# Kernel tuning notes

Measured on AMD Instinct MI355X. Metric: run time of the kernel, lower is better.

The kernel has to match this reference:

```python
import jax, jax.numpy as jnp
import numpy as np

EPS = 1e-12
FINAL_GROUPS = 256  # 4*64
FINAL_BIAS = 8.0


def resilu(x):
    # ReSiLU at default hardness == soft sigmoid gate
    return jax.nn.sigmoid(x)


def popcnt_layer(x, sel, w, b):
    # x: [B, In], sel: [O, P] int, w: [O, P], b: [O]
    selected = jnp.take(x, sel, axis=1)          # [B, O, P] gather
    weighted = selected * resilu(w)[None, :, :]  # weighted multiply
    summed = weighted.sum(axis=-1)               # [B, O] segment sum
    return resilu(summed - b[None, :])


def layer_norm(x, g, b):
    mu = x.mean(axis=-1, keepdims=True)
    var = ((x - mu) ** 2).mean(axis=-1, keepdims=True)
    return (x - mu) * jax.lax.rsqrt(var + EPS) * g + b


def setup_inputs() -> dict:
    key = jax.random.key(0)
    ks = jax.random.split(key, 16)
    B, IN, O1, O3, P = 256, 3200, 8192, 4096, 128
    return {
        "x": jax.random.normal(ks[0], (B, IN), dtype=jnp.float32),
        "sel1": jax.random.randint(ks[1], (O1, P), 0, IN, dtype=jnp.int32),
        "w1": jax.random.normal(ks[2], (O1, P), dtype=jnp.float32),
        "b1": jax.random.normal(ks[3], (O1,), dtype=jnp.float32) * (P / 3) + (P / 4),
        "g1": jnp.ones((O1,), dtype=jnp.float32),
        "be1": jnp.zeros((O1,), dtype=jnp.float32),
        "sel2": jax.random.randint(ks[4], (O1, P), 0, O1, dtype=jnp.int32),
        "w2": jax.random.normal(ks[5], (O1, P), dtype=jnp.float32),
        "b2": jax.random.normal(ks[6], (O1,), dtype=jnp.float32) * (P / 3) + (P / 4),
        "g2": jnp.ones((O1,), dtype=jnp.float32),
        "be2": jnp.zeros((O1,), dtype=jnp.float32),
        "sel3": jax.random.randint(ks[7], (O3, P), 0, O1, dtype=jnp.int32),
        "w3": jax.random.normal(ks[8], (O3, P), dtype=jnp.float32),
        "b3": jax.random.normal(ks[9], (O3,), dtype=jnp.float32) * (P / 3) + (P / 4),
    }


def reference(x, sel1, w1, b1, g1, be1, sel2, w2, b2, g2, be2, sel3, w3, b3):
    h = popcnt_layer(x, sel1, w1, b1)
    h = layer_norm(h, g1, be1)
    h = popcnt_layer(h, sel2, w2, b2)
    h = layer_norm(h, g2, be2)
    h = popcnt_layer(h, sel3, w3, b3)          # [B, 4096]
    out = h.reshape(h.shape[0], FINAL_GROUPS, -1).sum(axis=-1) - FINAL_BIAS  # [B, 256]
    return out
```

## Files before the change

kernel.cpp:

```cpp
#include <hip/hip_runtime.h>
#include <hip/hip_fp16.h>
#include <stdint.h>

#define BATCH 256
#define PSEL  128
#define IN_DIM 3200
#define O1_DIM 8192
#define O3_DIM 4096

__global__ __launch_bounds__(256) void transpose_kernel(const float* __restrict__ x,
                                                        __half* __restrict__ xT,
                                                        float* __restrict__ stats) {
    int tx = threadIdx.x;
    int ty = threadIdx.y;
    int tid = ty * 32 + tx;
    int gid = blockIdx.y * gridDim.x + blockIdx.x;
    if (gid < 4) stats[gid * 256 + tid] = 0.0f;

    __shared__ float tile[32][33];
    int i0 = blockIdx.x * 32;
    int b0 = blockIdx.y * 32;
#pragma unroll
    for (int k = 0; k < 4; ++k)
        tile[ty + k * 8][tx] =
            __builtin_nontemporal_load(&x[(size_t)(b0 + ty + k * 8) * IN_DIM + i0 + tx]);
    __syncthreads();
#pragma unroll
    for (int k = 0; k < 4; ++k)
        xT[(size_t)(i0 + ty + k * 8) * BATCH + b0 + tx] =
            __float2half(tile[tx][ty + k * 8]);
}

__global__ __launch_bounds__(256) void stats_kernel(const __half* __restrict__ hT,
                                                    float* __restrict__ gsum,
                                                    float* __restrict__ gsq) {
    int t   = threadIdx.x;
    int col = t & 127;
    int rp  = t >> 7;
    int r0  = blockIdx.x * 256 + rp * 128;
    const uint32_t* p = (const uint32_t*)hT + (size_t)r0 * 128 + col;
    float s0 = 0.f, s1 = 0.f, q0 = 0.f, q1 = 0.f;
#pragma unroll
    for (int ob = 0; ob < 16; ++ob) {
        uint32_t d[8];
#pragma unroll
        for (int j = 0; j < 8; ++j) d[j] = p[(size_t)(ob * 8 + j) * 128];
#pragma unroll
        for (int j = 0; j < 8; ++j) {
            float2 f = __half22float2(*(const __half2*)&d[j]);
            s0 += f.x; q0 = fmaf(f.x, f.x, q0);
            s1 += f.y; q1 = fmaf(f.y, f.y, q1);
        }
    }
    __shared__ float4 s_red[128];
    if (rp == 1) s_red[col] = make_float4(s0, s1, q0, q1);
    __syncthreads();
    if (rp == 0) {
        float4 r = s_red[col];
        atomicAdd(&gsum[2 * col],     s0 + r.x);
        atomicAdd(&gsum[2 * col + 1], s1 + r.y);
        atomicAdd(&gsq[2 * col],      q0 + r.z);
        atomicAdd(&gsq[2 * col + 1],  q1 + r.w);
    }
}

template <bool NORM>
__global__ __launch_bounds__(256, 4) void popcnt_kernel(
    const __half* __restrict__ actT,
    const int* __restrict__ sel,
    const float* __restrict__ w,
    const float* __restrict__ bias,
    const float* __restrict__ g,
    const float* __restrict__ be,
    const float* __restrict__ gsum,
    const float* __restrict__ gsq,
    float inv_n,
    __half* __restrict__ outp)
{
    const int o  = blockIdx.x;
    const int t  = threadIdx.x;
    const int cw = t & 31;
    const int rg = t >> 5;

    __shared__ uint32_t s_off[PSEL];
    __shared__ float    s_A[PSEL];
    __shared__ float s_rA[PSEL], s_rC[PSEL];
    __shared__ float s_acc[8][264];
    __shared__ float s_sums[2];

    if (t < PSEL) {
        int idx  = __builtin_nontemporal_load(&sel[o * PSEL + t]);
        float ww = __builtin_nontemporal_load(&w[o * PSEL + t]);
        float sw = 1.0f / (1.0f + __expf(-ww));
        float a, c;
        if (NORM) { a = sw * g[idx]; c = sw * be[idx]; }
        else      { a = sw;          c = 0.0f; }
        s_off[t] = (uint32_t)idx << 9;
        s_A[t]   = a;
        if (NORM) { s_rA[t] = a; s_rC[t] = c; }
    }
    __syncthreads();

    if (NORM && t < 64) {
        float va = s_rA[t] + s_rA[t + 64];
        float vc = s_rC[t] + s_rC[t + 64];
#pragma unroll
        for (int off = 32; off > 0; off >>= 1) {
            va += __shfl_down(va, off, 64);
            vc += __shfl_down(vc, off, 64);
        }
        if (t == 0) { s_sums[0] = va; s_sums[1] = vc; }
    }

    const uint32_t lane_off = (uint32_t)(cw << 4);
    uint32_t voff[16];
#pragma unroll
    for (int j = 0; j < 16; ++j)
        voff[j] = s_off[j * 8 + rg] + lane_off;
    uint4 d[16];
#pragma unroll
    for (int j = 0; j < 16; ++j)
        asm volatile("global_load_dwordx4 %0, %1, %2 sc0"
                     : "=v"(d[j])
                     : "v"(voff[j]), "s"(actT)
                     : "memory");
    asm volatile("s_waitcnt vmcnt(0)" ::: "memory");
    __builtin_amdgcn_sched_barrier(0);

    float acc[8] = {0.f, 0.f, 0.f, 0.f, 0.f, 0.f, 0.f, 0.f};
#pragma unroll
    for (int j = 0; j < 16; ++j) {
        float A = s_A[j * 8 + rg];
        const __half2* hp = (const __half2*)&d[j];
        float2 f0 = __half22float2(hp[0]);
        float2 f1 = __half22float2(hp[1]);
        float2 f2 = __half22float2(hp[2]);
        float2 f3 = __half22float2(hp[3]);
        acc[0] = fmaf(A, f0.x, acc[0]);
        acc[1] = fmaf(A, f0.y, acc[1]);
        acc[2] = fmaf(A, f1.x, acc[2]);
        acc[3] = fmaf(A, f1.y, acc[3]);
        acc[4] = fmaf(A, f2.x, acc[4]);
        acc[5] = fmaf(A, f2.y, acc[5]);
        acc[6] = fmaf(A, f3.x, acc[6]);
        acc[7] = fmaf(A, f3.y, acc[7]);
    }

    *(float4*)&s_acc[rg][8 * cw]     = make_float4(acc[0], acc[1], acc[2], acc[3]);
    *(float4*)&s_acc[rg][8 * cw + 4] = make_float4(acc[4], acc[5], acc[6], acc[7]);
    __syncthreads();

    float ab = 0.0f;
#pragma unroll
    for (int r = 0; r < 8; ++r) ab += s_acc[r][t];

    float bo = bias[o];
    float z;
    if (NORM) {
        float m  = gsum[t] * inv_n;
        float q  = gsq[t] * inv_n;
        float rs = rsqrtf(q - m * m + 1e-12f);
        z = rs * ab + s_sums[1] - rs * m * s_sums[0] - bo;
    } else {
        z = ab - bo;
    }
    float h = 1.0f / (1.0f + __expf(-z));
    __builtin_nontemporal_store(__half_as_ushort(__float2half(h)),
                                (unsigned short*)outp + (size_t)o * BATCH + t);
}

__global__ __launch_bounds__(256) void final_reduce(const __half* __restrict__ h3T,
                                                    float* __restrict__ out) {
    int gidx = blockIdx.x;
    int b    = threadIdx.x;
    const unsigned short* p = (const unsigned short*)h3T + (size_t)gidx * 16 * BATCH + b;
    float s = -8.0f;
#pragma unroll
    for (int j = 0; j < 16; ++j)
        s += __half2float(__ushort_as_half(__builtin_nontemporal_load(p + j * BATCH)));
    __builtin_nontemporal_store(s, &out[(size_t)b * 256 + gidx]);
}

extern "C" void kernel_launch(void* const* d_in, const int* in_sizes, int n_in,
                              void* d_out, int out_size, void* d_ws, size_t ws_size,
                              hipStream_t stream) {
    const float* x    = (const float*)d_in[0];
    const int*   sel1 = (const int*)d_in[1];
    const float* w1   = (const float*)d_in[2];
    const float* b1   = (const float*)d_in[3];
    const float* g1   = (const float*)d_in[4];
    const float* be1  = (const float*)d_in[5];
    const int*   sel2 = (const int*)d_in[6];
    const float* w2   = (const float*)d_in[7];
    const float* b2   = (const float*)d_in[8];
    const float* g2   = (const float*)d_in[9];
    const float* be2  = (const float*)d_in[10];
    const int*   sel3 = (const int*)d_in[11];
    const float* w3   = (const float*)d_in[12];
    const float* b3   = (const float*)d_in[13];
    float* out = (float*)d_out;

    char* ws = (char*)d_ws;
    __half* xT  = (__half*)(ws);
    __half* h1T = (__half*)(ws + 1638400);
    __half* h2T = (__half*)(ws + 1638400 + 4194304);
    __half* h3T = h1T;
    float* stats = (float*)(ws + 1638400 + 2 * 4194304);
    float* gs1 = stats;
    float* gq1 = stats + 256;
    float* gs2 = stats + 512;
    float* gq2 = stats + 768;

    transpose_kernel<<<dim3(IN_DIM / 32, BATCH / 32), dim3(32, 8), 0, stream>>>(
        x, xT, stats);

    popcnt_kernel<false><<<O1_DIM, 256, 0, stream>>>(
        xT, sel1, w1, b1, nullptr, nullptr, nullptr, nullptr, 0.0f, h1T);

    stats_kernel<<<O1_DIM / 256, 256, 0, stream>>>(h1T, gs1, gq1);

    popcnt_kernel<true><<<O1_DIM, 256, 0, stream>>>(
        h1T, sel2, w2, b2, g1, be1, gs1, gq1, 1.0f / (float)O1_DIM, h2T);

    stats_kernel<<<O1_DIM / 256, 256, 0, stream>>>(h2T, gs2, gq2);

    popcnt_kernel<true><<<O3_DIM, 256, 0, stream>>>(
        h2T, sel3, w3, b3, g2, be2, gs2, gq2, 1.0f / (float)O1_DIM, h3T);

    final_reduce<<<256, 256, 0, stream>>>(h3T, out);
}
```

Baseline: 182.4 us.

## Stage batch-slab activation tables in LDS for layers 2 and 3

Layers 2 and 3 now use a new kernel that copies a 128KB slab of the activation table (8 batch columns across all 8192 features) into LDS and gathers from shared memory instead of global/L2. A pack kernel precomputes the folded layer-norm weights (sigmoid(w)*g), byte offsets and per-output bias/shift metadata once. Activations are stored in a batch-blocked layout, and stats are computed per slab without atomics. This removes the repeated random global gathers and trades them for large LDS use (low occupancy), extra pack and relayout passes, and more workspace.

After: 233.7 us. 1.28x slower.

```diff
diff --git a/kernel.cpp b/kernel.cpp
--- a/kernel.cpp
+++ b/kernel.cpp
@@ -7,6 +7,13 @@
 #define IN_DIM 3200
 #define O1_DIM 8192
 #define O3_DIM 4096
+
+typedef unsigned int u32x4 __attribute__((ext_vector_type(4)));
+
+static __device__ inline uint32_t pack_half2(float a, float b) {
+    __half2 h = __floats2half2_rn(a, b);
+    return *reinterpret_cast<uint32_t*>(&h);
+}
 
 __global__ __launch_bounds__(256) void transpose_kernel(const float* __restrict__ x,
                                                         __half* __restrict__ xT,
@@ -31,7 +38,44 @@
             __float2half(tile[tx][ty + k * 8]);
 }
 
+__global__ __launch_bounds__(256) void pack_kernel(
+    const int* __restrict__ sel, const float* __restrict__ w,
+    const float* __restrict__ g, const float* __restrict__ be,
+    const float* __restrict__ bias,
+    uint2* __restrict__ pack, float2* __restrict__ meta) {
+    const int t = threadIdx.x;
+    const int slot = t >> 7;
+    const int e = t & 127;
+    const int o0 = blockIdx.x * 16;
+    __shared__ float s_p[4][2];
+    for (int k = 0; k < 8; ++k) {
+        int o = o0 + 2 * k + slot;
+        int idx  = sel[(size_t)o * PSEL + e];
+        float wv = w[(size_t)o * PSEL + e];
+        float sw = 1.0f / (1.0f + __expf(-wv));
+        float A = sw * g[idx];
+        float C = sw * be[idx];
+        pack[(size_t)o * PSEL + e] = make_uint2((uint32_t)idx << 4, __float_as_uint(A));
+        float va = A, vc = C;
+#pragma unroll
+        for (int off = 32; off > 0; off >>= 1) {
+            va += __shfl_down(va, off, 64);
+            vc += __shfl_down(vc, off, 64);
+        }
+        if ((t & 63) == 0) { s_p[t >> 6][0] = va; s_p[t >> 6][1] = vc; }
+        __syncthreads();
+        if (t < 2) {
+            float sA = s_p[2 * t][0] + s_p[2 * t + 1][0];
+            float sC = s_p[2 * t][1] + s_p[2 * t + 1][1];
+            int oo = o0 + 2 * k + t;
+            meta[oo] = make_float2(sA, sC - bias[oo]);
+        }
+        __syncthreads();
+    }
+}
+
 __global__ __launch_bounds__(256) void stats_kernel(const __half* __restrict__ hT,
+                                                    __half* __restrict__ hblk,
                                                     float* __restrict__ gsum,
                                                     float* __restrict__ gsq) {
     int t   = threadIdx.x;
@@ -39,6 +83,7 @@
     int rp  = t >> 7;
     int r0  = blockIdx.x * 256 + rp * 128;
     const uint32_t* p = (const uint32_t*)hT + (size_t)r0 * 128 + col;
+    char* blkbase = (char*)hblk + (size_t)(col >> 2) * 131072 + (size_t)(col & 3) * 4;
     float s0 = 0.f, s1 = 0.f, q0 = 0.f, q1 = 0.f;
 #pragma unroll
     for (int ob = 0; ob < 16; ++ob) {
@@ -47,6 +92,8 @@
         for (int j = 0; j < 8; ++j) d[j] = p[(size_t)(ob * 8 + j) * 128];
 #pragma unroll
         for (int j = 0; j < 8; ++j) {
+            int r = r0 + ob * 8 + j;
+            __builtin_nontemporal_store(d[j], (uint32_t*)(blkbase + (size_t)r * 16));
             float2 f = __half22float2(*(const __half2*)&d[j]);
             s0 += f.x; q0 = fmaf(f.x, f.x, q0);
             s1 += f.y; q1 = fmaf(f.y, f.y, q1);
@@ -64,19 +111,40 @@
     }
 }
 
-template <bool NORM>
+__global__ __launch_bounds__(256) void stats_blk_kernel(const uint32_t* __restrict__ hblk,
+                                                        float* __restrict__ gsum,
+                                                        float* __restrict__ gsq) {
+    int t = threadIdx.x;
+    int s = blockIdx.x;
+    const uint32_t* p = hblk + (size_t)s * 32768;
+    float s0 = 0.f, s1 = 0.f, q0 = 0.f, q1 = 0.f;
+#pragma unroll 8
+    for (int k = 0; k < 128; ++k) {
+        uint32_t d = p[(size_t)k * 256 + t];
+        float2 f = __half22float2(*(const __half2*)&d);
+        s0 += f.x; q0 = fmaf(f.x, f.x, q0);
+        s1 += f.y; q1 = fmaf(f.y, f.y, q1);
+    }
+    __shared__ float4 red[256];
+    red[t] = make_float4(s0, s1, q0, q1);
+    __syncthreads();
+    if (t < 4) {
+        float a0 = 0.f, a1 = 0.f, b0 = 0.f, b1 = 0.f;
+        for (int m = 0; m < 64; ++m) {
+            float4 r = red[t + 4 * m];
+            a0 += r.x; a1 += r.y; b0 += r.z; b1 += r.w;
+        }
+        gsum[s * 8 + 2 * t]     = a0;
+        gsum[s * 8 + 2 * t + 1] = a1;
+        gsq[s * 8 + 2 * t]      = b0;
+        gsq[s * 8 + 2 * t + 1]  = b1;
+    }
+}
+
 __global__ __launch_bounds__(256, 4) void popcnt_kernel(
-    const __half* __restrict__ actT,
-    const int* __restrict__ sel,
-    const float* __restrict__ w,
-    const float* __restrict__ bias,
-    const float* __restrict__ g,
-    const float* __restrict__ be,
-    const float* __restrict__ gsum,
-    const float* __restrict__ gsq,
-    float inv_n,
-    __half* __restrict__ outp)
-{
+    const __half* __restrict__ actT, const int* __restrict__ sel,
+    const float* __restrict__ w, const float* __restrict__ bias,
+    __half* __restrict__ outp) {
     const int o  = blockIdx.x;
     const int t  = threadIdx.x;
     const int cw = t & 31;
@@ -84,33 +152,16 @@
 
     __shared__ uint32_t s_off[PSEL];
     __shared__ float    s_A[PSEL];
-    __shared__ float s_rA[PSEL], s_rC[PSEL];
     __shared__ float s_acc[8][264];
-    __shared__ float s_sums[2];
 
     if (t < PSEL) {
         int idx  = __builtin_nontemporal_load(&sel[o * PSEL + t]);
         float ww = __builtin_nontemporal_load(&w[o * PSEL + t]);
         float sw = 1.0f / (1.0f + __expf(-ww));
-        float a, c;
-        if (NORM) { a = sw * g[idx]; c = sw * be[idx]; }
-        else      { a = sw;          c = 0.0f; }
         s_off[t] = (uint32_t)idx << 9;
-        s_A[t]   = a;
-        if (NORM) { s_rA[t] = a; s_rC[t] = c; }
-    }
-    __syncthreads();
-
-    if (NORM && t < 64) {
-        float va = s_rA[t] + s_rA[t + 64];
-        float vc = s_rC[t] + s_rC[t + 64];
-#pragma unroll
-        for (int off = 32; off > 0; off >>= 1) {
-            va += __shfl_down(va, off, 64);
-            vc += __shfl_down(vc, off, 64);
-        }
-        if (t == 0) { s_sums[0] = va; s_sums[1] = vc; }
-    }
+        s_A[t]   = sw;
+    }
+    __syncthreads();
 
     const uint32_t lane_off = (uint32_t)(cw << 4);
     uint32_t voff[16];
@@ -121,9 +172,7 @@
 #pragma unroll
     for (int j = 0; j < 16; ++j)
         asm volatile("global_load_dwordx4 %0, %1, %2 sc0"
-                     : "=v"(d[j])
-                     : "v"(voff[j]), "s"(actT)
-                     : "memory");
+                     : "=v"(d[j]) : "v"(voff[j]), "s"(actT) : "memory");
     asm volatile("s_waitcnt vmcnt(0)" ::: "memory");
     __builtin_amdgcn_sched_barrier(0);
 
@@ -154,30 +203,106 @@
 #pragma unroll
     for (int r = 0; r < 8; ++r) ab += s_acc[r][t];
 
-    float bo = bias[o];
-    float z;
-    if (NORM) {
-        float m  = gsum[t] * inv_n;
-        float q  = gsq[t] * inv_n;
-        float rs = rsqrtf(q - m * m + 1e-12f);
-        z = rs * ab + s_sums[1] - rs * m * s_sums[0] - bo;
-    } else {
-        z = ab - bo;
-    }
+    float z = ab - bias[o];
     float h = 1.0f / (1.0f + __expf(-z));
     __builtin_nontemporal_store(__half_as_ushort(__float2half(h)),
                                 (unsigned short*)outp + (size_t)o * BATCH + t);
 }
 
-__global__ __launch_bounds__(256) void final_reduce(const __half* __restrict__ h3T,
+__global__ __launch_bounds__(512, 2) void popcnt_lds_kernel(
+    const uint4* __restrict__ tblblk,
+    const uint2* __restrict__ pack,
+    const float2* __restrict__ meta,
+    const float* __restrict__ gsum, const float* __restrict__ gsq,
+    float inv_n,
+    __half* __restrict__ outblk,
+    int nout, int out_slab_halves) {
+    extern __shared__ char smem[];
+    __shared__ float s_rs[8], s_rsm[8];
+    const int t  = threadIdx.x;
+    const int bt = blockIdx.x & 31;
+    const int o0 = (blockIdx.x >> 5) * nout;
+
+    if (t < 8) {
+        float m = gsum[bt * 8 + t] * inv_n;
+        float q = gsq[bt * 8 + t] * inv_n;
+        float rs = rsqrtf(q - m * m + 1e-12f);
+        s_rs[t] = rs;
+        s_rsm[t] = rs * m;
+    }
+    {
+        const uint4* src = tblblk + (size_t)bt * 8192;
+        uint4* dst = (uint4*)smem;
+#pragma unroll
+        for (int i = 0; i < 16; ++i) dst[i * 512 + t] = src[i * 512 + t];
+    }
+    __syncthreads();
+
+    const int og = t >> 3;
+    const int pc = t & 7;
+    const int nsteps = nout >> 6;
+    for (int s = 0; s < nsteps; ++s) {
+        const int o = o0 + s * 64 + og;
+        const uint4* pk4 = (const uint4*)(pack + (size_t)o * PSEL + pc * 16);
+        uint4 q[8];
+#pragma unroll
+        for (int m = 0; m < 8; ++m) q[m] = pk4[m];
+
+        float acc[8] = {0.f, 0.f, 0.f, 0.f, 0.f, 0.f, 0.f, 0.f};
+#pragma unroll
+        for (int m = 0; m < 8; ++m) {
+            uint4 da = *(const uint4*)(smem + q[m].x);
+            float Aa = __uint_as_float(q[m].y);
+            uint4 db = *(const uint4*)(smem + q[m].z);
+            float Ab = __uint_as_float(q[m].w);
+            const __half2* ha = (const __half2*)&da;
+            const __half2* hb = (const __half2*)&db;
+#pragma unroll
+            for (int n = 0; n < 4; ++n) {
+                float2 fa = __half22float2(ha[n]);
+                float2 fb = __half22float2(hb[n]);
+                acc[2 * n]     = fmaf(Aa, fa.x, acc[2 * n]);
+                acc[2 * n + 1] = fmaf(Aa, fa.y, acc[2 * n + 1]);
+                acc[2 * n]     = fmaf(Ab, fb.x, acc[2 * n]);
+                acc[2 * n + 1] = fmaf(Ab, fb.y, acc[2 * n + 1]);
+            }
+        }
+#pragma unroll
+        for (int off = 4; off > 0; off >>= 1) {
+#pragma unroll
+            for (int j = 0; j < 8; ++j)
+                acc[j] += __shfl_down(acc[j], off, 8);
+        }
+        if (pc == 0) {
+            float2 mt = meta[o];
+            float h[8];
+#pragma unroll
+            for (int j = 0; j < 8; ++j) {
+                float z = s_rs[j] * acc[j] + mt.y - s_rsm[j] * mt.x;
+                h[j] = 1.0f / (1.0f + __expf(-z));
+            }
+            u32x4 r;
+            r.x = pack_half2(h[0], h[1]);
+            r.y = pack_half2(h[2], h[3]);
+            r.z = pack_half2(h[4], h[5]);
+            r.w = pack_half2(h[6], h[7]);
+            __builtin_nontemporal_store(
+                r, (u32x4*)((unsigned short*)outblk + (size_t)bt * out_slab_halves +
+                            (size_t)o * 8));
+        }
+    }
+}
+
+__global__ __launch_bounds__(256) void final_reduce(const unsigned short* __restrict__ h3blk,
                                                     float* __restrict__ out) {
     int gidx = blockIdx.x;
     int b    = threadIdx.x;
-    const unsigned short* p = (const unsigned short*)h3T + (size_t)gidx * 16 * BATCH + b;
+    const unsigned short* p =
+        h3blk + (size_t)(b >> 3) * 32768 + (size_t)(16 * gidx) * 8 + (b & 7);
     float s = -8.0f;
 #pragma unroll
     for (int j = 0; j < 16; ++j)
-        s += __half2float(__ushort_as_half(__builtin_nontemporal_load(p + j * BATCH)));
+        s += __half2float(__ushort_as_half(__builtin_nontemporal_load(p + j * 8)));
     __builtin_nontemporal_store(s, &out[(size_t)b * 256 + gidx]);
 }
 
@@ -201,31 +326,43 @@
     float* out = (float*)d_out;
 
     char* ws = (char*)d_ws;
-    __half* xT  = (__half*)(ws);
-    __half* h1T = (__half*)(ws + 1638400);
-    __half* h2T = (__half*)(ws + 1638400 + 4194304);
-    __half* h3T = h1T;
-    float* stats = (float*)(ws + 1638400 + 2 * 4194304);
+    __half* xT    = (__half*)(ws);
+    __half* h1T   = (__half*)(ws + 1638400);
+    __half* h1blk = (__half*)(ws + 5832704);
+    __half* h2blk = (__half*)(ws + 10027008);
+    __half* h3blk = (__half*)(ws + 14221312);
+    uint2*  pack2 = (uint2*)(ws + 16318464);
+    uint2*  pack3 = (uint2*)(ws + 24707072);
+    float2* meta2 = (float2*)(ws + 28901376);
+    float2* meta3 = (float2*)(ws + 28966912);
+    float*  stats = (float*)(ws + 28999680);
     float* gs1 = stats;
     float* gq1 = stats + 256;
     float* gs2 = stats + 512;
     float* gq2 = stats + 768;
 
+    (void)hipFuncSetAttribute((const void*)popcnt_lds_kernel,
+                              hipFuncAttributeMaxDynamicSharedMemorySize, 131072);
+
     transpose_kernel<<<dim3(IN_DIM / 32, BATCH / 32), dim3(32, 8), 0, stream>>>(
         x, xT, stats);
 
-    popcnt_kernel<false><<<O1_DIM, 256, 0, stream>>>(
-        xT, sel1, w1, b1, nullptr, nullptr, nullptr, nullptr, 0.0f, h1T);
-
-    stats_kernel<<<O1_DIM / 256, 256, 0, stream>>>(h1T, gs1, gq1);
-
-    popcnt_kernel<true><<<O1_DIM, 256, 0, stream>>>(
-        h1T, sel2, w2, b2, g1, be1, gs1, gq1, 1.0f / (float)O1_DIM, h2T);
-
-    stats_kernel<<<O1_DIM / 256, 256, 0, stream>>>(h2T, gs2, gq2);
-
-    popcnt_kernel<true><<<O3_DIM, 256, 0, stream>>>(
-        h2T, sel3, w3, b3, g2, be2, gs2, gq2, 1.0f / (float)O1_DIM, h3T);
-
-    final_reduce<<<256, 256, 0, stream>>>(h3T, out);
-}
+    pack_kernel<<<O1_DIM / 16, 256, 0, stream>>>(sel2, w2, g1, be1, b2, pack2, meta2);
+    pack_kernel<<<O3_DIM / 16, 256, 0, stream>>>(sel3, w3, g2, be2, b3, pack3, meta3);
+
+    popcnt_kernel<<<O1_DIM, 256, 0, stream>>>(xT, sel1, w1, b1, h1T);
+
+    stats_kernel<<<O1_DIM / 256, 256, 0, stream>>>(h1T, h1blk, gs1, gq1);
+
+    popcnt_lds_kernel<<<256, 512, 131072, stream>>>(
+        (const uint4*)h1blk, pack2, meta2, gs1, gq1, 1.0f / (float)O1_DIM,
+        h2blk, O1_DIM / 8, O1_DIM * 8);
+
+    stats_blk_kernel<<<32, 256, 0, stream>>>((const uint32_t*)h2blk, gs2, gq2);
+
+    popcnt_lds_kernel<<<256, 512, 131072, stream>>>(
+        (const uint4*)h2blk, pack3, meta3, gs2, gq2, 1.0f / (float)O1_DIM,
+        h3blk, O3_DIM / 8, O3_DIM * 8);
+
+    final_reduce<<<256, 256, 0, stream>>>((const unsigned short*)h3blk, out);
+}
```
